# Kernel tuning notes

Hardware: AMD Instinct MI355X
Metric: run time of the kernel (lower is better)

Reference implementation:

```python
import jax, jax.numpy as jnp
import numpy as np

LN_EPS = 1e-5

def _lstm_cell(x, h, c, Wih, Whh, bih, bhh):
    # gates: [b, 4*d], PyTorch LSTMCell gate order: i, f, g, o
    gates = x @ Wih.T + bih + h @ Whh.T + bhh
    i, f, g, o = jnp.split(gates, 4, axis=-1)
    c_new = jax.nn.sigmoid(f) * c + jax.nn.sigmoid(i) * jnp.tanh(g)
    h_new = jax.nn.sigmoid(o) * jnp.tanh(c_new)
    return h_new, c_new

def _layernorm(x, g, b):
    mu = jnp.mean(x, axis=-1, keepdims=True)
    var = jnp.mean(jnp.square(x - mu), axis=-1, keepdims=True)
    return (x - mu) * jax.lax.rsqrt(var + LN_EPS) * g + b

def setup_inputs() -> dict:
    key = jax.random.key(0)
    ks = jax.random.split(key, 8)
    B, F_, L, D, V, NL = 128, 1, 32, 512, 10000, 2
    features = jax.random.normal(ks[0], (B, F_, D), dtype=jnp.float32)
    caption = jax.random.randint(ks[1], (B, L), 0, V, dtype=jnp.int64)
    emb_W = jax.random.normal(ks[2], (V, D), dtype=jnp.float32) * 0.02
    W_ih = jax.random.normal(ks[3], (NL, 4 * D, D), dtype=jnp.float32) * (1.0 / np.sqrt(D))
    W_hh = jax.random.normal(ks[4], (NL, 4 * D, D), dtype=jnp.float32) * (1.0 / np.sqrt(D))
    b_ih = jnp.zeros((NL, 4 * D), dtype=jnp.float32)
    b_hh = jnp.zeros((NL, 4 * D), dtype=jnp.float32)
    ln_g = jnp.ones((D,), dtype=jnp.float32)
    ln_b = jnp.zeros((D,), dtype=jnp.float32)
    fc_W = jax.random.normal(ks[5], (V, D), dtype=jnp.float32) * np.sqrt(2.0 / D)
    fc_b = jnp.zeros((V,), dtype=jnp.float32)
    return {"features": features, "caption": caption, "emb_W": emb_W,
            "W_ih": W_ih, "W_hh": W_hh, "b_ih": b_ih, "b_hh": b_hh,
            "ln_g": ln_g, "ln_b": ln_b, "fc_W": fc_W, "fc_b": fc_b}

def reference(features, caption, emb_W, W_ih, W_hh, b_ih, b_hh, ln_g, ln_b, fc_W, fc_b):
    b, f, d = features.shape
    n_layers = W_ih.shape[0]
    emb = emb_W[caption]                                   # [b, L, d]
    inp = jnp.concatenate([features, emb], axis=1)         # [b, T, d], T = f + L
    h0 = jnp.zeros((b, d), dtype=features.dtype)
    c0 = jnp.zeros((b, d), dtype=features.dtype)

    def step(carry, x_t):
        h, c = carry
        # Faithful to the original: every layer consumes x_t, sharing (h, c).
        for l in range(n_layers):
            h, c = _lstm_cell(x_t, h, c, W_ih[l], W_hh[l], b_ih[l], b_hh[l])
        h = _layernorm(h, ln_g, ln_b)                      # normalized h carries forward
        logits_t = h @ fc_W.T + fc_b                       # [b, V]
        return (h, c), logits_t

    xs = jnp.swapaxes(inp, 0, 1)                           # [T, b, d]
    _, logits = jax.lax.scan(step, (h0, c0), xs)           # [T, b, V]
    logits = jnp.swapaxes(logits, 0, 1)                    # [b, T, V]
    return jax.nn.log_softmax(logits[:, f:, :], axis=-1)   # [b, L, V]
```

## Files before the change

### kernel.cpp

```cpp
#include <hip/hip_runtime.h>

#define B_ 128
#define D_ 512
#define T_ 33
#define L_ 32
#define V_ 10000
#define NWG 128
#define NHELP 128
#define THREADS 512
#define NTILE_M 32
#define NTILE_N 79

typedef short short8 __attribute__((ext_vector_type(8)));
typedef float f32x4 __attribute__((ext_vector_type(4)));
typedef unsigned uint32x4 __attribute__((ext_vector_type(4)));
typedef unsigned uint32x2 __attribute__((ext_vector_type(2)));

__device__ __forceinline__ short f2bf_rne(float f) {
    unsigned u = __builtin_bit_cast(unsigned, f);
    unsigned r = (u + 0x7FFFu + ((u >> 16) & 1u)) >> 16;
    return (short)r;
}
__device__ __forceinline__ void split2(float v, short& hi, short& lo) {
    unsigned u = __builtin_bit_cast(unsigned, v);
    hi = (short)(u >> 16);
    float hif = __builtin_bit_cast(float, u & 0xFFFF0000u);
    lo = (short)(__builtin_bit_cast(unsigned, v - hif) >> 16);
}
__device__ __forceinline__ float sigm(float x) {
    return 1.0f / (1.0f + __expf(-x));
}
__device__ __forceinline__ float unpack2f(unsigned u) {
    return __builtin_bit_cast(float, u << 16)
         + __builtin_bit_cast(float, u & 0xFFFF0000u);
}

__device__ __forceinline__ void llc_stu(void* p, unsigned v) {
    __hip_atomic_store((unsigned*)p, v, __ATOMIC_RELAXED,
                       __HIP_MEMORY_SCOPE_SYSTEM);
}
__device__ __forceinline__ uint32x4 llc_ld4(const void* p) {
    uint32x4 r;
    asm volatile("global_load_dwordx4 %0, %1, off sc0 sc1"
                 : "=v"(r) : "v"(p));
    return r;
}
__device__ __forceinline__ uint32x2 llc_ld2(const void* p) {
    uint32x2 r;
    asm volatile("global_load_dwordx2 %0, %1, off sc0 sc1"
                 : "=v"(r) : "v"(p));
    return r;
}
__device__ __forceinline__ void llc_wait() {
    asm volatile("s_waitcnt vmcnt(0)" ::: "memory");
    __builtin_amdgcn_sched_barrier(0);
}

__global__ void prep_kernel(const float* __restrict__ features,
                            const int* __restrict__ caption,
                            const float* __restrict__ embW,
                            const float* __restrict__ fcW,
                            short* __restrict__ Xhi,
                            short* __restrict__ Xlo,
                            short* __restrict__ fcWb,
                            int* __restrict__ syncv) {
    const long NX = (long)T_ * B_ * D_;
    const long NW = (long)V_ * D_;
    const long total = NX + NW;
    long gid = (long)blockIdx.x * blockDim.x + threadIdx.x;
    if (gid < NWG) syncv[gid] = 0;
    for (long idx = gid; idx < total; idx += (long)gridDim.x * blockDim.x) {
        if (idx < NX) {
            int t = (int)(idx / (B_ * D_));
            int r = (int)(idx % (B_ * D_));
            int b = r >> 9;
            int d = r & 511;
            float v;
            if (t == 0) v = features[r];
            else        v = embW[(long)caption[b * L_ + (t - 1)] * D_ + d];
            short hi, lo;
            split2(v, hi, lo);
            Xhi[idx] = hi;
            Xlo[idx] = lo;
        } else {
            long j = idx - NX;
            fcWb[j] = f2bf_rne(fcW[j]);
        }
    }
}

__global__ __launch_bounds__(THREADS)
void lstm_persist(const short* __restrict__ Xhi, const short* __restrict__ Xlo,
                  const float* __restrict__ Wih, const float* __restrict__ Whh,
                  const float* __restrict__ bih, const float* __restrict__ bhh,
                  const float* __restrict__ lng, const float* __restrict__ lnb,
                  unsigned* __restrict__ H0p, unsigned* __restrict__ H1p,
                  short* __restrict__ Hnb, int* __restrict__ syncv,
                  const short* __restrict__ fcWb, const float* __restrict__ fcb,
                  float* __restrict__ out) {
    __shared__ __align__(16) short Wh[2][16][1032];
    __shared__ __align__(16) short Wo[2][16][1032];
    __shared__ float gbuf[128][17];
    __shared__ float carr[128][4];
    __shared__ float rs_s[128], murs_s[128];
    __shared__ float gam_s[512], bet_s[512];
    __shared__ float bias_s[2][16];
    __shared__ float bconst_s[16];
    __shared__ float sgam_s[16];

    const int tid  = threadIdx.x;
    const int wave = tid >> 6;
    const int lane = tid & 63;
    int* flags = syncv;

    if (blockIdx.x >= NWG) {
        const int h = blockIdx.x - NWG;
        short* As = (short*)&Wh[0][0][0];
        short* Bs = As + 2 * 128 * 40;
        const int lrow  = tid >> 2;
        const int lcol  = (tid & 3) * 8;
        const int wavem = (wave >> 2) * 64;
        const int waven = (wave & 3) * 32;
        const int rsel  = lane & 15;
        const int kcol  = (lane >> 4) * 8;
        const int rquad = (lane >> 4) * 4;
        const int ncol  = lane & 15;

        for (int tau = h; tau < NTILE_M * NTILE_N; tau += NHELP) {
            const int mt = tau / NTILE_N;
            const int nt = tau - mt * NTILE_N;
            const int m0 = mt * 128, n0 = nt * 128;
            if (wave == 0) {
                const int tgt = 2 * mt + 5;
                int it2 = 0;
                for (;;) {
                    int f0 = __hip_atomic_load(&flags[lane], __ATOMIC_RELAXED,
                                               __HIP_MEMORY_SCOPE_SYSTEM);
                    int f1 = __hip_atomic_load(&flags[64 + lane], __ATOMIC_RELAXED,
                                               __HIP_MEMORY_SCOPE_SYSTEM);
                    if (__all(f0 >= tgt && f1 >= tgt)) break;
                    if (++it2 > (1 << 20)) break;
                    __builtin_amdgcn_s_sleep(8);
                }
            }
            __syncthreads();

            f32x4 acc[4][2];
            #pragma unroll
            for (int i = 0; i < 4; ++i)
                #pragma unroll
                for (int j = 0; j < 2; ++j)
                    acc[i][j] = (f32x4){0.f, 0.f, 0.f, 0.f};

            const short* Ab = Hnb + (long)(m0 + lrow) * D_ + lcol;
            const int nrow = n0 + lrow;
            const short* Bb = fcWb + (long)nrow * D_ + lcol;
            const bool bok = nrow < V_;

            uint32x4 va = llc_ld4(Ab);
            uint32x4 vb = 0;
            if (bok) vb = llc_ld4(Bb);
            llc_wait();
            *(uint32x4*)&As[lrow * 40 + lcol] = va;
            *(uint32x4*)&Bs[lrow * 40 + lcol] = vb;
            uint32x4 va2 = llc_ld4(Ab + 32);
            uint32x4 vb2 = 0;
            if (bok) vb2 = llc_ld4(Bb + 32);
            __syncthreads();

            for (int kc = 0; kc < 16; ++kc) {
                const int bo = (kc & 1) * 5120;
                short8 a[4], bw[2];
                #pragma unroll
                for (int i = 0; i < 4; ++i)
                    a[i] = *(const short8*)&As[bo + (wavem + i * 16 + rsel) * 40 + kcol];
                #pragma unroll
                for (int j = 0; j < 2; ++j)
                    bw[j] = *(const short8*)&Bs[bo + (waven + j * 16 + rsel) * 40 + kcol];
                #pragma unroll
                for (int i = 0; i < 4; ++i)
                    #pragma unroll
                    for (int j = 0; j < 2; ++j)
                        acc[i][j] = __builtin_amdgcn_mfma_f32_16x16x32_bf16(a[i], bw[j], acc[i][j], 0, 0, 0);
                if (kc + 1 < 16) {
                    llc_wait();
                    const int b1 = ((kc + 1) & 1) * 5120;
                    *(uint32x4*)&As[b1 + lrow * 40 + lcol] = va2;
                    *(uint32x4*)&Bs[b1 + lrow * 40 + lcol] = vb2;
                    if (kc + 2 < 16) {
                        va2 = llc_ld4(Ab + (kc + 2) * 32);
                        vb2 = 0;
                        if (bok) vb2 = llc_ld4(Bb + (kc + 2) * 32);
                    }
                }
                __syncthreads();
            }

            #pragma unroll
            for (int i = 0; i < 4; ++i) {
                #pragma unroll
                for (int j = 0; j < 2; ++j) {
                    const int ngl = n0 + waven + j * 16 + ncol;
                    if (ngl < V_) {
                        const float bv = fcb[ngl];
                        #pragma unroll
                        for (int r = 0; r < 4; ++r) {
                            const int mgl = m0 + wavem + i * 16 + rquad + r;
                            const int tt = mgl >> 7;
                            const int bb = mgl & 127;
                            out[((long)bb * L_ + tt) * V_ + ngl] = acc[i][j][r] + bv;
                        }
                    }
                }
            }
        }
        return;
    }

    const int w  = blockIdx.x;
    const int d0 = w * 4;
    const int wm = wave * 16;
    const int n  = lane & 15;
    const int kq = (lane >> 4) * 8;

    gam_s[tid & 511] = lng[tid & 511];
    bet_s[tid & 511] = lnb[tid & 511];
    if (tid < 32) {
        int l = tid >> 4, nn = tid & 15;
        int row = (nn >> 2) * 512 + d0 + (nn & 3);
        bias_s[l][nn] = bih[l * 2048 + row] + bhh[l * 2048 + row];
    }
    for (int idx = tid; idx < 2 * 16 * 1024; idx += THREADS) {
        int l = idx >> 14;
        int nn = (idx >> 10) & 15;
        int k = idx & 1023;
        int row = (nn >> 2) * 512 + d0 + (nn & 3);
        float v = (k < 512) ? Wih[((long)(l * 2048 + row)) * 512 + k]
                            : Whh[((long)(l * 2048 + row)) * 512 + (k - 512)];
        if (l == 0 && k >= 512) v *= lng[k - 512];
        short hi, lo;
        split2(v, hi, lo);
        Wh[l][nn][k] = hi;
        Wo[l][nn][k] = lo;
    }
    if (tid < 256) {
        const int c = tid >> 4, kc = tid & 15;
        const int row = (c >> 2) * 512 + d0 + (c & 3);
        float sb = 0.f, sg = 0.f;
        for (int k = kc * 32; k < kc * 32 + 32; ++k) {
            const float wv = Whh[(long)row * 512 + k];
            sb += lnb[k] * wv;
            sg += lng[k] * wv;
        }
        gbuf[c][kc]      = sb;
        gbuf[64 + c][kc] = sg;
    }
    carr[tid >> 2][tid & 3] = 0.f;
    __syncthreads();
    if (tid < 32) {
        const int c = tid & 15;
        const int base = (tid >= 16) ? 64 + c : c;
        float s = 0.f;
        for (int i = 0; i < 16; ++i) s += gbuf[base][i];
        if (tid < 16) bconst_s[c] = s;
        else          sgam_s[c]   = s;
    }
    __syncthreads();

    int nb = 0;

    auto arrive = [&]() {
        __syncthreads();
        ++nb;
        if (tid == 0)
            __hip_atomic_store(&flags[w], nb, __ATOMIC_RELAXED,
                               __HIP_MEMORY_SCOPE_SYSTEM);
    };
    auto wait_bar = [&]() {
        if (wave == 0) {
            const int tgt = nb;
            int iter = 0;
            for (;;) {
                int f0 = __hip_atomic_load(&flags[lane], __ATOMIC_RELAXED,
                                           __HIP_MEMORY_SCOPE_SYSTEM);
                int f1 = __hip_atomic_load(&flags[64 + lane], __ATOMIC_RELAXED,
                                           __HIP_MEMORY_SCOPE_SYSTEM);
                if (__all(f0 >= tgt && f1 >= tgt)) break;
                if (++iter > 65536) break;
                __builtin_amdgcn_s_sleep(1);
            }
        }
        __syncthreads();
    };

    auto ln_stats = [&]() {
        const int row = tid & 127, q = tid >> 7;
        const unsigned* hp = &H1p[row * 512 + q * 128];
        float s = 0.f, s2 = 0.f;
        #pragma unroll
        for (int c = 0; c < 2; ++c) {
            uint32x4 sb[16];
            #pragma unroll
            for (int i = 0; i < 16; ++i)
                sb[i] = llc_ld4(hp + c * 64 + i * 4);
            llc_wait();
            #pragma unroll
            for (int i = 0; i < 16; ++i) {
                #pragma unroll
                for (int e = 0; e < 4; ++e) {
                    const float v = unpack2f(sb[i][e]);
                    s  += v;
                    s2 += v * v;
                }
            }
        }
        gbuf[row][q * 2]     = s;
        gbuf[row][q * 2 + 1] = s2;
        __syncthreads();
        if (tid < 128) {
            const float ss  = gbuf[tid][0] + gbuf[tid][2] + gbuf[tid][4] + gbuf[tid][6];
            const float ss2 = gbuf[tid][1] + gbuf[tid][3] + gbuf[tid][5] + gbuf[tid][7];
            const float mu  = ss * (1.0f / 512.0f);
            const float var = ss2 * (1.0f / 512.0f) - mu * mu;
            const float rs  = rsqrtf(var + 1e-5f);
            rs_s[tid]   = rs;
            murs_s[tid] = mu * rs;
        }
        __syncthreads();
    };

    unsigned* Hnb32 = (unsigned*)Hnb;
    auto mat_slot = [&](int slot) {
        const int rb = w * 4;
        const int p0 = tid, p1 = tid + 512;
        const int m0r = rb + (p0 >> 8), k0 = (p0 & 255) * 2;
        const int m1r = rb + (p1 >> 8), k1 = (p1 & 255) * 2;
        uint32x2 a = llc_ld2(&H1p[m0r * 512 + k0]);
        uint32x2 b = llc_ld2(&H1p[m1r * 512 + k1]);
        llc_wait();
        {
            const float v0 = unpack2f(a[0]), v1 = unpack2f(a[1]);
            const float o0 = fmaf(fmaf(v0, rs_s[m0r], -murs_s[m0r]), gam_s[k0],     bet_s[k0]);
            const float o1 = fmaf(fmaf(v1, rs_s[m0r], -murs_s[m0r]), gam_s[k0 + 1], bet_s[k0 + 1]);
            const unsigned pk = (unsigned)(unsigned short)f2bf_rne(o0)
                              | ((unsigned)(unsigned short)f2bf_rne(o1) << 16);
            llc_stu(&Hnb32[((long)slot * B_ + m0r) * 256 + (p0 & 255)], pk);
        }
        {
            const float v0 = unpack2f(b[0]), v1 = unpack2f(b[1]);
            const float o0 = fmaf(fmaf(v0, rs_s[m1r], -murs_s[m1r]), gam_s[k1],     bet_s[k1]);
            const float o1 = fmaf(fmaf(v1, rs_s[m1r], -murs_s[m1r]), gam_s[k1 + 1], bet_s[k1 + 1]);
            const unsigned pk = (unsigned)(unsigned short)f2bf_rne(o0)
                              | ((unsigned)(unsigned short)f2bf_rne(o1) << 16);
            llc_stu(&Hnb32[((long)slot * B_ + m1r) * 256 + (p1 & 255)], pk);
        }
    };

    const int rA0 = (wm + n) * 512;
    const int rq  = (lane >> 4) * 4;

    for (int t = 0; t < T_; ++t) {
        const short* xh = Xhi + (long)t * B_ * D_;
        const short* xl = Xlo + (long)t * B_ * D_;

        {
            f32x4 accx = {0.f, 0.f, 0.f, 0.f};
            f32x4 acch = {0.f, 0.f, 0.f, 0.f};
            #pragma unroll 4
            for (int kc = 0; kc < 16; ++kc) {
                const int kg = kc * 32 + kq;
                short8 bh = *(const short8*)&Wh[0][n][kg];
                short8 bl = *(const short8*)&Wo[0][n][kg];
                short8 ah = *(const short8*)&xh[rA0 + kg];
                short8 al = *(const short8*)&xl[rA0 + kg];
                accx = __builtin_amdgcn_mfma_f32_16x16x32_bf16(ah, bh, accx, 0, 0, 0);
                accx = __builtin_amdgcn_mfma_f32_16x16x32_bf16(ah, bl, accx, 0, 0, 0);
                accx = __builtin_amdgcn_mfma_f32_16x16x32_bf16(al, bh, accx, 0, 0, 0);
            }
            if (t > 0) {
                wait_bar();
                #pragma unroll
                for (int half = 0; half < 2; ++half) {
                    uint32x4 hb[16];
                    #pragma unroll
                    for (int i = 0; i < 8; ++i) {
                        const int kh = (half * 8 + i) * 32 + kq;
                        hb[i * 2]     = llc_ld4(&H1p[rA0 + kh]);
                        hb[i * 2 + 1] = llc_ld4(&H1p[rA0 + kh + 4]);
                    }
                    llc_wait();
                    #pragma unroll
                    for (int i = 0; i < 8; ++i) {
                        const int kh = (half * 8 + i) * 32 + kq;
                        short8 bh = *(const short8*)&Wh[0][n][512 + kh];
                        short8 bl = *(const short8*)&Wo[0][n][512 + kh];
                        unsigned u[8];
                        *(uint32x4*)&u[0] = hb[i * 2];
                        *(uint32x4*)&u[4] = hb[i * 2 + 1];
                        short8 ah, al;
                        #pragma unroll
                        for (int j = 0; j < 8; ++j) {
                            ah[j] = (short)(u[j] & 0xFFFFu);
                            al[j] = (short)(u[j] >> 16);
                        }
                        acch = __builtin_amdgcn_mfma_f32_16x16x32_bf16(ah, bh, acch, 0, 0, 0);
                        acch = __builtin_amdgcn_mfma_f32_16x16x32_bf16(ah, bl, acch, 0, 0, 0);
                        acch = __builtin_amdgcn_mfma_f32_16x16x32_bf16(al, bh, acch, 0, 0, 0);
                    }
                }
                ln_stats();
                if (w < 32 && t >= 2) mat_slot(t - 2);
            }
            const float bs = bias_s[0][n] + (t > 0 ? bconst_s[n] : 0.f);
            const float sg = sgam_s[n];
            #pragma unroll
            for (int r = 0; r < 4; ++r) {
                const int row = wm + rq + r;
                float g = accx[r] + bs;
                if (t > 0) g += acch[r] * rs_s[row] - murs_s[row] * sg;
                gbuf[row][n] = g;
            }
            __syncthreads();
            {
                const int m = tid >> 2, d = tid & 3;
                const float gi = gbuf[m][d],     gf = gbuf[m][4 + d];
                const float gg = gbuf[m][8 + d], go = gbuf[m][12 + d];
                const float cn = sigm(gf) * carr[m][d] + sigm(gi) * tanhf(gg);
                carr[m][d] = cn;
                const float hv = sigm(go) * tanhf(cn);
                short hi_, lo_;
                split2(hv, hi_, lo_);
                const unsigned pk = (unsigned)(unsigned short)hi_
                                  | ((unsigned)(unsigned short)lo_ << 16);
                llc_stu(&H0p[m * 512 + d0 + d], pk);
            }
            arrive();
        }

        {
            f32x4 acc = {0.f, 0.f, 0.f, 0.f};
            #pragma unroll 4
            for (int kc = 0; kc < 16; ++kc) {
                const int kg = kc * 32 + kq;
                short8 bh = *(const short8*)&Wh[1][n][kg];
                short8 bl = *(const short8*)&Wo[1][n][kg];
                short8 ah = *(const short8*)&xh[rA0 + kg];
                short8 al = *(const short8*)&xl[rA0 + kg];
                acc = __builtin_amdgcn_mfma_f32_16x16x32_bf16(ah, bh, acc, 0, 0, 0);
                acc = __builtin_amdgcn_mfma_f32_16x16x32_bf16(ah, bl, acc, 0, 0, 0);
                acc = __builtin_amdgcn_mfma_f32_16x16x32_bf16(al, bh, acc, 0, 0, 0);
            }
            wait_bar();
            #pragma unroll
            for (int half = 0; half < 2; ++half) {
                uint32x4 hb[16];
                #pragma unroll
                for (int i = 0; i < 8; ++i) {
                    const int kh = (half * 8 + i) * 32 + kq;
                    hb[i * 2]     = llc_ld4(&H0p[rA0 + kh]);
                    hb[i * 2 + 1] = llc_ld4(&H0p[rA0 + kh + 4]);
                }
                llc_wait();
                #pragma unroll
                for (int i = 0; i < 8; ++i) {
                    const int kh = (half * 8 + i) * 32 + kq;
                    short8 bh = *(const short8*)&Wh[1][n][512 + kh];
                    short8 bl = *(const short8*)&Wo[1][n][512 + kh];
                    unsigned u[8];
                    *(uint32x4*)&u[0] = hb[i * 2];
                    *(uint32x4*)&u[4] = hb[i * 2 + 1];
                    short8 ah, al;
                    #pragma unroll
                    for (int j = 0; j < 8; ++j) {
                        ah[j] = (short)(u[j] & 0xFFFFu);
                        al[j] = (short)(u[j] >> 16);
                    }
                    acc = __builtin_amdgcn_mfma_f32_16x16x32_bf16(ah, bh, acc, 0, 0, 0);
                    acc = __builtin_amdgcn_mfma_f32_16x16x32_bf16(ah, bl, acc, 0, 0, 0);
                    acc = __builtin_amdgcn_mfma_f32_16x16x32_bf16(al, bh, acc, 0, 0, 0);
                }
            }
            const float bs = bias_s[1][n];
            #pragma unroll
            for (int r = 0; r < 4; ++r)
                gbuf[wm + rq + r][n] = acc[r] + bs;
            __syncthreads();
            {
                const int m = tid >> 2, d = tid & 3;
                const float gi = gbuf[m][d],     gf = gbuf[m][4 + d];
                const float gg = gbuf[m][8 + d], go = gbuf[m][12 + d];
                const float cn = sigm(gf) * carr[m][d] + sigm(gi) * tanhf(gg);
                carr[m][d] = cn;
                const float hv = sigm(go) * tanhf(cn);
                short hi_, lo_;
                split2(hv, hi_, lo_);
                const unsigned pk = (unsigned)(unsigned short)hi_
                                  | ((unsigned)(unsigned short)lo_ << 16);
                llc_stu(&H1p[m * 512 + d0 + d], pk);
            }
            arrive();
        }
    }

    wait_bar();
    ln_stats();
    if (w < 32) mat_slot(L_ - 1);
    arrive();
}

__global__ void logsoftmax_kernel(float* __restrict__ out) {
    __shared__ float red[256];
    const long row = blockIdx.x;
    float* p = out + row * V_;
    float4* p4 = reinterpret_cast<float4*>(p);
    const int tid = threadIdx.x;
    float s = 0.f;
    for (int i = tid; i < V_ / 4; i += 256) {
        float4 v = p4[i];
        s += __expf(v.x) + __expf(v.y) + __expf(v.z) + __expf(v.w);
    }
    red[tid] = s;
    __syncthreads();
    for (int st = 128; st > 0; st >>= 1) {
        if (tid < st) red[tid] += red[tid + st];
        __syncthreads();
    }
    const float ls = logf(red[0]);
    for (int i = tid; i < V_ / 4; i += 256) {
        float4 v = p4[i];
        v.x -= ls; v.y -= ls; v.z -= ls; v.w -= ls;
        p4[i] = v;
    }
}

extern "C" void kernel_launch(void* const* d_in, const int* in_sizes, int n_in,
                              void* d_out, int out_size, void* d_ws, size_t ws_size,
                              hipStream_t stream) {
    const float* features = (const float*)d_in[0];
    const int*   caption  = (const int*)d_in[1];
    const float* embW     = (const float*)d_in[2];
    const float* W_ih     = (const float*)d_in[3];
    const float* W_hh     = (const float*)d_in[4];
    const float* b_ih     = (const float*)d_in[5];
    const float* b_hh     = (const float*)d_in[6];
    const float* ln_g     = (const float*)d_in[7];
    const float* ln_b     = (const float*)d_in[8];
    const float* fc_W     = (const float*)d_in[9];
    const float* fc_b     = (const float*)d_in[10];
    float* out = (float*)d_out;

    char* ws = (char*)d_ws;
    int*      syncv = (int*)ws;      ws += 512;
    short*    Xhi   = (short*)ws;    ws += (size_t)T_ * B_ * D_ * 2;
    short*    Xlo   = (short*)ws;    ws += (size_t)T_ * B_ * D_ * 2;
    unsigned* H0p   = (unsigned*)ws; ws += (size_t)B_ * D_ * 4;
    unsigned* H1p   = (unsigned*)ws; ws += (size_t)B_ * D_ * 4;
    short*    Hnb   = (short*)ws;    ws += (size_t)L_ * B_ * D_ * 2;
    short*    fcWb  = (short*)ws;    ws += (size_t)V_ * D_ * 2;

    prep_kernel<<<2048, 256, 0, stream>>>(features, caption, embW, fc_W,
                                          Xhi, Xlo, fcWb, syncv);

    lstm_persist<<<NWG + NHELP, THREADS, 0, stream>>>(
        Xhi, Xlo, W_ih, W_hh, b_ih, b_hh, ln_g, ln_b,
        H0p, H1p, Hnb, syncv, fcWb, fc_b, out);

    logsoftmax_kernel<<<4096, 256, 0, stream>>>(out);
}
```

Baseline: 1.802 ms.

## Fuse LayerNorm stats into recurrent matmul and overlap hidden-state loads

Issues all 32 hidden-state loads up front and waits with vmcnt(16), so the second half's loads overlap the first half's MFMAs. LayerNorm mean and variance are now accumulated from the same loaded values inside the recurrent matmul and reduced with wave shuffles, which removes the separate ln_stats pass that re-read H1 and did an extra block-wide reduction. The fcW loads in the helper GEMM switch from LLC-bypassing loads to ordinary cached loads, and the helper's polling sleep is made longer. The cost is higher register pressure from 32 live vector loads, and the wave-local stats assume each wave covers full rows.

```diff
diff --git a/kernel.cpp b/kernel.cpp
--- a/kernel.cpp
+++ b/kernel.cpp
@@ -51,8 +51,12 @@
                  : "=v"(r) : "v"(p));
     return r;
 }
-__device__ __forceinline__ void llc_wait() {
+__device__ __forceinline__ void llc_wait0() {
     asm volatile("s_waitcnt vmcnt(0)" ::: "memory");
+    __builtin_amdgcn_sched_barrier(0);
+}
+__device__ __forceinline__ void llc_wait16() {
+    asm volatile("s_waitcnt vmcnt(16)" ::: "memory");
     __builtin_amdgcn_sched_barrier(0);
 }
 
@@ -140,7 +144,7 @@
                                                __HIP_MEMORY_SCOPE_SYSTEM);
                     if (__all(f0 >= tgt && f1 >= tgt)) break;
                     if (++it2 > (1 << 20)) break;
-                    __builtin_amdgcn_s_sleep(8);
+                    __builtin_amdgcn_s_sleep(32);
                 }
             }
             __syncthreads();
@@ -158,14 +162,12 @@
             const bool bok = nrow < V_;
 
             uint32x4 va = llc_ld4(Ab);
-            uint32x4 vb = 0;
-            if (bok) vb = llc_ld4(Bb);
-            llc_wait();
+            uint32x4 vb = bok ? *(const uint32x4*)Bb : (uint32x4)0;
+            llc_wait0();
             *(uint32x4*)&As[lrow * 40 + lcol] = va;
             *(uint32x4*)&Bs[lrow * 40 + lcol] = vb;
             uint32x4 va2 = llc_ld4(Ab + 32);
-            uint32x4 vb2 = 0;
-            if (bok) vb2 = llc_ld4(Bb + 32);
+            uint32x4 vb2 = bok ? *(const uint32x4*)(Bb + 32) : (uint32x4)0;
             __syncthreads();
 
             for (int kc = 0; kc < 16; ++kc) {
@@ -183,14 +185,13 @@
                     for (int j = 0; j < 2; ++j)
                         acc[i][j] = __builtin_amdgcn_mfma_f32_16x16x32_bf16(a[i], bw[j], acc[i][j], 0, 0, 0);
                 if (kc + 1 < 16) {
-                    llc_wait();
+                    llc_wait0();
                     const int b1 = ((kc + 1) & 1) * 5120;
                     *(uint32x4*)&As[b1 + lrow * 40 + lcol] = va2;
                     *(uint32x4*)&Bs[b1 + lrow * 40 + lcol] = vb2;
                     if (kc + 2 < 16) {
                         va2 = llc_ld4(Ab + (kc + 2) * 32);
-                        vb2 = 0;
-                        if (bok) vb2 = llc_ld4(Bb + (kc + 2) * 32);
+                        vb2 = bok ? *(const uint32x4*)(Bb + (kc + 2) * 32) : (uint32x4)0;
                     }
                 }
                 __syncthreads();
@@ -303,7 +304,7 @@
             #pragma unroll
             for (int i = 0; i < 16; ++i)
                 sb[i] = llc_ld4(hp + c * 64 + i * 4);
-            llc_wait();
+            llc_wait0();
             #pragma unroll
             for (int i = 0; i < 16; ++i) {
                 #pragma unroll
@@ -337,7 +338,7 @@
         const int m1r = rb + (p1 >> 8), k1 = (p1 & 255) * 2;
         uint32x2 a = llc_ld2(&H1p[m0r * 512 + k0]);
         uint32x2 b = llc_ld2(&H1p[m1r * 512 + k1]);
-        llc_wait();
+        llc_wait0();
         {
             const float v0 = unpack2f(a[0]), v1 = unpack2f(a[1]);
             const float o0 = fmaf(fmaf(v0, rs_s[m0r], -murs_s[m0r]), gam_s[k0],     bet_s[k0]);
@@ -379,36 +380,74 @@
             }
             if (t > 0) {
                 wait_bar();
-                #pragma unroll
-                for (int half = 0; half < 2; ++half) {
-                    uint32x4 hb[16];
+                uint32x4 hb0[16], hb1[16];
+                #pragma unroll
+                for (int i = 0; i < 8; ++i) {
+                    const int kh = i * 32 + kq;
+                    hb0[i * 2]     = llc_ld4(&H1p[rA0 + kh]);
+                    hb0[i * 2 + 1] = llc_ld4(&H1p[rA0 + kh + 4]);
+                }
+                #pragma unroll
+                for (int i = 0; i < 8; ++i) {
+                    const int kh = (8 + i) * 32 + kq;
+                    hb1[i * 2]     = llc_ld4(&H1p[rA0 + kh]);
+                    hb1[i * 2 + 1] = llc_ld4(&H1p[rA0 + kh + 4]);
+                }
+                float s = 0.f, s2 = 0.f;
+                llc_wait16();
+                #pragma unroll
+                for (int i = 0; i < 8; ++i) {
+                    const int kh = i * 32 + kq;
+                    short8 bh = *(const short8*)&Wh[0][n][512 + kh];
+                    short8 bl = *(const short8*)&Wo[0][n][512 + kh];
+                    unsigned u[8];
+                    *(uint32x4*)&u[0] = hb0[i * 2];
+                    *(uint32x4*)&u[4] = hb0[i * 2 + 1];
+                    short8 ah, al;
                     #pragma unroll
-                    for (int i = 0; i < 8; ++i) {
-                        const int kh = (half * 8 + i) * 32 + kq;
-                        hb[i * 2]     = llc_ld4(&H1p[rA0 + kh]);
-                        hb[i * 2 + 1] = llc_ld4(&H1p[rA0 + kh + 4]);
+                    for (int j = 0; j < 8; ++j) {
+                        ah[j] = (short)(u[j] & 0xFFFFu);
+                        al[j] = (short)(u[j] >> 16);
+                        const float v = unpack2f(u[j]);
+                        s  += v;
+                        s2 += v * v;
                     }
-                    llc_wait();
+                    acch = __builtin_amdgcn_mfma_f32_16x16x32_bf16(ah, bh, acch, 0, 0, 0);
+                    acch = __builtin_amdgcn_mfma_f32_16x16x32_bf16(ah, bl, acch, 0, 0, 0);
+                    acch = __builtin_amdgcn_mfma_f32_16x16x32_bf16(al, bh, acch, 0, 0, 0);
+                }
+                llc_wait0();
+                #pragma unroll
+                for (int i = 0; i < 8; ++i) {
+                    const int kh = (8 + i) * 32 + kq;
+                    short8 bh = *(const short8*)&Wh[0][n][512 + kh];
+                    short8 bl = *(const short8*)&Wo[0][n][512 + kh];
+                    unsigned u[8];
+                    *(uint32x4*)&u[0] = hb1[i * 2];
+                    *(uint32x4*)&u[4] = hb1[i * 2 + 1];
+                    short8 ah, al;
                     #pragma unroll
-                    for (int i = 0; i < 8; ++i) {
-                        const int kh = (half * 8 + i) * 32 + kq;
-                        short8 bh = *(const short8*)&Wh[0][n][512 + kh];
-                        short8 bl = *(const short8*)&Wo[0][n][512 + kh];
-                        unsigned u[8];
-                        *(uint32x4*)&u[0] = hb[i * 2];
-                        *(uint32x4*)&u[4] = hb[i * 2 + 1];
-                        short8 ah, al;
-                        #pragma unroll
-                        for (int j = 0; j < 8; ++j) {
-                            ah[j] = (short)(u[j] & 0xFFFFu);
-                            al[j] = (short)(u[j] >> 16);
-                        }
-                        acch = __builtin_amdgcn_mfma_f32_16x16x32_bf16(ah, bh, acch, 0, 0, 0);
-                        acch = __builtin_amdgcn_mfma_f32_16x16x32_bf16(ah, bl, acch, 0, 0, 0);
-                        acch = __builtin_amdgcn_mfma_f32_16x16x32_bf16(al, bh, acch, 0, 0, 0);
+                    for (int j = 0; j < 8; ++j) {
+                        ah[j] = (short)(u[j] & 0xFFFFu);
+                        al[j] = (short)(u[j] >> 16);
+                        const float v = unpack2f(u[j]);
+                        s  += v;
+                        s2 += v * v;
                     }
-                }
-                ln_stats();
+                    acch = __builtin_amdgcn_mfma_f32_16x16x32_bf16(ah, bh, acch, 0, 0, 0);
+                    acch = __builtin_amdgcn_mfma_f32_16x16x32_bf16(ah, bl, acch, 0, 0, 0);
+                    acch = __builtin_amdgcn_mfma_f32_16x16x32_bf16(al, bh, acch, 0, 0, 0);
+                }
+                s  += __shfl_xor(s, 16);  s  += __shfl_xor(s, 32);
+                s2 += __shfl_xor(s2, 16); s2 += __shfl_xor(s2, 32);
+                if (lane < 16) {
+                    const float mu  = s * (1.0f / 512.0f);
+                    const float var = s2 * (1.0f / 512.0f) - mu * mu;
+                    const float rs  = rsqrtf(var + 1e-5f);
+                    rs_s[wm + lane]   = rs;
+                    murs_s[wm + lane] = mu * rs;
+                }
+                __syncthreads();
                 if (w < 32 && t >= 2) mat_slot(t - 2);
             }
             const float bs = bias_s[0][n] + (t > 0 ? bconst_s[n] : 0.f);
@@ -451,24 +490,48 @@
                 acc = __builtin_amdgcn_mfma_f32_16x16x32_bf16(al, bh, acc, 0, 0, 0);
             }
             wait_bar();
-            #pragma unroll
-            for (int half = 0; half < 2; ++half) {
-                uint32x4 hb[16];
-                #pragma unroll
-                for (int i = 0; i < 8; ++i) {
-                    const int kh = (half * 8 + i) * 32 + kq;
-                    hb[i * 2]     = llc_ld4(&H0p[rA0 + kh]);
-                    hb[i * 2 + 1] = llc_ld4(&H0p[rA0 + kh + 4]);
-                }
-                llc_wait();
-                #pragma unroll
-                for (int i = 0; i < 8; ++i) {
-                    const int kh = (half * 8 + i) * 32 + kq;
+            {
+                uint32x4 hb0[16], hb1[16];
+                #pragma unroll
+                for (int i = 0; i < 8; ++i) {
+                    const int kh = i * 32 + kq;
+                    hb0[i * 2]     = llc_ld4(&H0p[rA0 + kh]);
+                    hb0[i * 2 + 1] = llc_ld4(&H0p[rA0 + kh + 4]);
+                }
+                #pragma unroll
+                for (int i = 0; i < 8; ++i) {
+                    const int kh = (8 + i) * 32 + kq;
+                    hb1[i * 2]     = llc_ld4(&H0p[rA0 + kh]);
+                    hb1[i * 2 + 1] = llc_ld4(&H0p[rA0 + kh + 4]);
+                }
+                llc_wait16();
+                #pragma unroll
+                for (int i = 0; i < 8; ++i) {
+                    const int kh = i * 32 + kq;
                     short8 bh = *(const short8*)&Wh[1][n][512 + kh];
                     short8 bl = *(const short8*)&Wo[1][n][512 + kh];
                     unsigned u[8];
-                    *(uint32x4*)&u[0] = hb[i * 2];
-                    *(uint32x4*)&u[4] = hb[i * 2 + 1];
+                    *(uint32x4*)&u[0] = hb0[i * 2];
+                    *(uint32x4*)&u[4] = hb0[i * 2 + 1];
+                    short8 ah, al;
+                    #pragma unroll
+                    for (int j = 0; j < 8; ++j) {
+                        ah[j] = (short)(u[j] & 0xFFFFu);
+                        al[j] = (short)(u[j] >> 16);
+                    }
+                    acc = __builtin_amdgcn_mfma_f32_16x16x32_bf16(ah, bh, acc, 0, 0, 0);
+                    acc = __builtin_amdgcn_mfma_f32_16x16x32_bf16(ah, bl, acc, 0, 0, 0);
+                    acc = __builtin_amdgcn_mfma_f32_16x16x32_bf16(al, bh, acc, 0, 0, 0);
+                }
+                llc_wait0();
+                #pragma unroll
+                for (int i = 0; i < 8; ++i) {
+                    const int kh = (8 + i) * 32 + kq;
+                    short8 bh = *(const short8*)&Wh[1][n][512 + kh];
+                    short8 bl = *(const short8*)&Wo[1][n][512 + kh];
+                    unsigned u[8];
+                    *(uint32x4*)&u[0] = hb1[i * 2];
+                    *(uint32x4*)&u[4] = hb1[i * 2 + 1];
                     short8 ah, al;
                     #pragma unroll
                     for (int j = 0; j < 8; ++j) {
```

Measured after the change: 1.771 ms. Within noise of the previous version (-1.7%).
